# Optimization experiments

Measured on AMD Instinct MI355X. Metric: run time of the kernel, lower is better.

The kernel has to match this reference:

```python
import jax, jax.numpy as jnp
import numpy as np

SEQ_LEN = 4096
INPUT_DIM = 768
DIM = 512
NUM_HEADS = 8
HEAD_DIM = DIM // NUM_HEADS
WINDOW_SIZE = 7
DILATION = 8
HALF_WINDOW = WINDOW_SIZE // 2  # 3
BIDIRECTIONAL = True


def _dilated_mask(seq_len):
    # allowed neighbors of query i: j = i + k*DILATION for k in [-HALF_WINDOW, HALF_WINDOW]
    # (only k<=0 if not bidirectional), clipped to [0, seq_len)
    idx = jnp.arange(seq_len)
    d = idx[None, :] - idx[:, None]  # j - i
    allowed = (d % DILATION == 0) & (jnp.abs(d) <= DILATION * HALF_WINDOW)
    if not BIDIRECTIONAL:
        allowed = allowed & (d <= 0)
    return jnp.where(allowed, 0.0, -jnp.inf).astype(jnp.float32)  # [S, S]


def setup_inputs() -> dict:
    key = jax.random.key(0)
    ks = jax.random.split(key, 6)
    s = 0.02
    return {
        "x": jax.random.normal(ks[0], (SEQ_LEN, INPUT_DIM), dtype=jnp.float32),
        "W_in": jax.random.normal(ks[1], (INPUT_DIM, DIM), dtype=jnp.float32) * s,
        "b_in": jnp.zeros((DIM,), dtype=jnp.float32),
        "W_tse": jax.random.normal(ks[2], (DIM, 3 * DIM), dtype=jnp.float32) * s,
        "W_out": jax.random.normal(ks[3], (DIM, DIM), dtype=jnp.float32) * s,
        "b_out": jnp.zeros((DIM,), dtype=jnp.float32),
    }


def reference(x, W_in, b_in, W_tse, W_out, b_out):
    S = x.shape[0]
    scale = HEAD_DIM ** -0.5
    h = x @ W_in + b_in                                   # [S, DIM]
    tse = (h @ W_tse).reshape(S, 3, NUM_HEADS, HEAD_DIM)   # [S, 3, H, hd]
    q, k, v = tse[:, 0], tse[:, 1], tse[:, 2]              # each [S, H, hd]
    scores = jnp.einsum("shd,thd->hst", q, k) * scale      # [H, S, S]
    scores = scores + _dilated_mask(S)[None, :, :]
    attn = jax.nn.softmax(scores, axis=-1)                 # [H, S, S]
    out = jnp.einsum("hst,thd->shd", attn, v)              # [S, H, hd]
    out = out.reshape(S, DIM)
    return out @ W_out + b_out                              # [S, DIM]
```

## Files before the change

kernel.cpp:

```cpp
#include <hip/hip_runtime.h>
#include <hip/hip_bf16.h>

#define S_LEN 4096
#define IN_DIM 768
#define D_DIM 512
#define N_HEADS 8
#define H_DIM 64
#define TSE_DIM 1536

typedef __attribute__((ext_vector_type(8))) short frag8;
typedef __attribute__((ext_vector_type(4))) float f32x4;

__device__ __forceinline__ unsigned short f2bfbits(float f) {
    unsigned int u = __float_as_uint(f);
    unsigned int r = (u + 0x7FFFu + ((u >> 16) & 1u)) >> 16;
    return (unsigned short)r;
}
__device__ __forceinline__ float bf2f(unsigned short b) {
    return __uint_as_float(((unsigned int)b) << 16);
}

__device__ __forceinline__ void gload_lds16(const void* g, void* l) {
    __builtin_amdgcn_global_load_lds(
        (const __attribute__((address_space(1))) unsigned int*)g,
        (__attribute__((address_space(3))) unsigned int*)l,
        16, 0, 0);
}

__global__ __launch_bounds__(256) void prep_kernel(
        const float4* __restrict__ x4, ushort4* __restrict__ xb4,
        const float* __restrict__ W_in,  unsigned short* __restrict__ WinT,
        const float* __restrict__ W_tse, unsigned short* __restrict__ WtseT,
        const float* __restrict__ W_out, unsigned short* __restrict__ WoutT) {
    __shared__ float tile[32][33];
    int b = blockIdx.x;
    if (b < 3072) {
        int i = b * 256 + threadIdx.x;
        float4 v = x4[i];
        ushort4 o;
        o.x = f2bfbits(v.x); o.y = f2bfbits(v.y);
        o.z = f2bfbits(v.z); o.w = f2bfbits(v.w);
        xb4[i] = o;
        return;
    }
    const float* in; unsigned short* out; int K, N, t;
    if (b < 3456)      { t = b - 3072; in = W_in;  out = WinT;  K = IN_DIM; N = D_DIM;  }
    else if (b < 4224) { t = b - 3456; in = W_tse; out = WtseT; K = D_DIM;  N = TSE_DIM;}
    else               { t = b - 4224; in = W_out; out = WoutT; K = D_DIM;  N = D_DIM;  }
    int ktiles = K / 32;
    int kb = (t % ktiles) * 32, nb = (t / ktiles) * 32;
    int tx = threadIdx.x & 31, ty = threadIdx.x >> 5;
    #pragma unroll
    for (int r = ty; r < 32; r += 8)
        tile[r][tx] = in[(size_t)(kb + r) * N + nb + tx];
    __syncthreads();
    #pragma unroll
    for (int r = ty; r < 32; r += 8)
        out[(size_t)(nb + r) * K + kb + tx] = f2bfbits(tile[tx][r]);
}

template<int K, bool OUT_BF16, bool BIAS>
__global__ __launch_bounds__(256) void gemm_nt(
        const unsigned short* __restrict__ A,
        const unsigned short* __restrict__ Bt,
        const float* __restrict__ bias,
        void* __restrict__ C,
        int M, int N) {
    constexpr int NT = K >> 5;
    constexpr int NP = NT >> 1;
    __shared__ __align__(16) unsigned short As[4][64 * 32];
    __shared__ __align__(16) unsigned short Bs[4][64 * 32];

    const int bm = blockIdx.x * 64;
    const int bn = blockIdx.y * 64;
    const int lane = threadIdx.x & 63;
    const int wave = threadIdx.x >> 6;
    const int wr = wave >> 1;
    const int wc = wave & 1;
    const int fr = lane & 15;
    const int fg = lane >> 4;

    const int srow = lane >> 2;
    const int scol = (lane & 3) * 8;

    const unsigned short* agp = A  + (size_t)(bm + wave * 16 + srow) * K + scol;
    const unsigned short* bgp = Bt + (size_t)(bn + wave * 16 + srow) * K + scol;

    f32x4 acc[2][2];
    #pragma unroll
    for (int mi = 0; mi < 2; ++mi)
        #pragma unroll
        for (int ni = 0; ni < 2; ++ni)
            acc[mi][ni] = (f32x4)(0.f);

    #define STAGE(t, b)                                          \
        gload_lds16(agp + (t) * 32, &As[b][wave * 512]);         \
        gload_lds16(bgp + (t) * 32, &Bs[b][wave * 512]);

    #define COMPUTE(b)                                                           \
        {                                                                        \
            frag8 a_[2], b_[2];                                                  \
            _Pragma("unroll")                                                    \
            for (int mi = 0; mi < 2; ++mi)                                       \
                a_[mi] = *(const frag8*)&As[b][(wr * 32 + mi * 16 + fr) * 32 + fg * 8]; \
            _Pragma("unroll")                                                    \
            for (int ni = 0; ni < 2; ++ni)                                       \
                b_[ni] = *(const frag8*)&Bs[b][(wc * 32 + ni * 16 + fr) * 32 + fg * 8]; \
            _Pragma("unroll")                                                    \
            for (int mi = 0; mi < 2; ++mi)                                       \
                _Pragma("unroll")                                                \
                for (int ni = 0; ni < 2; ++ni)                                   \
                    acc[mi][ni] = __builtin_amdgcn_mfma_f32_16x16x32_bf16(       \
                            a_[mi], b_[ni], acc[mi][ni], 0, 0, 0);               \
        }

    STAGE(0, 0)
    STAGE(1, 1)
    __syncthreads();

    #pragma unroll
    for (int p = 0; p < NP; ++p) {
        const int s0 = (p & 1) * 2;
        if (p + 1 < NP) {
            const int s1 = ((p + 1) & 1) * 2;
            STAGE(2 * p + 2, s1 + 0)
            STAGE(2 * p + 3, s1 + 1)
        }
        COMPUTE(s0 + 0)
        COMPUTE(s0 + 1)
        if (p + 1 < NP) __syncthreads();
    }
    #undef STAGE
    #undef COMPUTE

    #pragma unroll
    for (int mi = 0; mi < 2; ++mi) {
        int grow = bm + wr * 32 + mi * 16 + fg * 4;
        #pragma unroll
        for (int ni = 0; ni < 2; ++ni) {
            int gcol = bn + wc * 32 + ni * 16 + fr;
            float bv = BIAS ? bias[gcol] : 0.f;
            #pragma unroll
            for (int r = 0; r < 4; ++r) {
                float v = acc[mi][ni][r] + bv;
                if (OUT_BF16)
                    ((unsigned short*)C)[(size_t)(grow + r) * N + gcol] = f2bfbits(v);
                else
                    ((float*)C)[(size_t)(grow + r) * N + gcol] = v;
            }
        }
    }
}

__global__ __launch_bounds__(256) void attn_kernel(
        const unsigned short* __restrict__ tse, unsigned short* __restrict__ out) {
    const int s    = blockIdx.x * 4 + (threadIdx.x >> 6);
    const int lane = threadIdx.x & 63;
    const int off  = (lane >> 3) * H_DIM + (lane & 7) * 8;

    float qf[8];
    {
        frag8 q = *(const frag8*)(tse + (size_t)s * TSE_DIM + off);
        #pragma unroll
        for (int i = 0; i < 8; ++i) qf[i] = bf2f((unsigned short)q[i]);
    }

    float sc[7];
    #pragma unroll
    for (int j = 0; j < 7; ++j) {
        int t = s + (j - 3) * 8;
        bool valid = (t >= 0) && (t < S_LEN);
        float p = 0.f;
        if (valid) {
            frag8 k = *(const frag8*)(tse + (size_t)t * TSE_DIM + D_DIM + off);
            #pragma unroll
            for (int i = 0; i < 8; ++i) p += qf[i] * bf2f((unsigned short)k[i]);
        }
        p += __shfl_xor(p, 1, 64);
        p += __shfl_xor(p, 2, 64);
        p += __shfl_xor(p, 4, 64);
        sc[j] = valid ? p * 0.125f : -__builtin_inff();
    }

    float m = sc[0];
    #pragma unroll
    for (int j = 1; j < 7; ++j) m = fmaxf(m, sc[j]);

    float w[7], denom = 0.f;
    #pragma unroll
    for (int j = 0; j < 7; ++j) {
        w[j] = (sc[j] == -__builtin_inff()) ? 0.f : __expf(sc[j] - m);
        denom += w[j];
    }
    const float inv = 1.f / denom;

    float of[8];
    #pragma unroll
    for (int i = 0; i < 8; ++i) of[i] = 0.f;
    #pragma unroll
    for (int j = 0; j < 7; ++j) {
        int t = s + (j - 3) * 8;
        if (t >= 0 && t < S_LEN) {
            frag8 v = *(const frag8*)(tse + (size_t)t * TSE_DIM + 2 * D_DIM + off);
            #pragma unroll
            for (int i = 0; i < 8; ++i) of[i] += w[j] * bf2f((unsigned short)v[i]);
        }
    }

    frag8 o;
    #pragma unroll
    for (int i = 0; i < 8; ++i) o[i] = (short)f2bfbits(of[i] * inv);
    *(frag8*)(out + (size_t)s * D_DIM + off) = o;
}

extern "C" void kernel_launch(void* const* d_in, const int* in_sizes, int n_in,
                              void* d_out, int out_size, void* d_ws, size_t ws_size,
                              hipStream_t stream) {
    (void)in_sizes; (void)n_in; (void)out_size;
    const float* x     = (const float*)d_in[0];
    const float* W_in  = (const float*)d_in[1];
    const float* b_in  = (const float*)d_in[2];
    const float* W_tse = (const float*)d_in[3];
    const float* W_out = (const float*)d_in[4];
    const float* b_out = (const float*)d_in[5];

    char* p = (char*)d_ws;
    unsigned short* xb    = (unsigned short*)p; p += (size_t)S_LEN * IN_DIM * 2;
    unsigned short* WinT  = (unsigned short*)p; p += (size_t)D_DIM * IN_DIM * 2;
    unsigned short* WtseT = (unsigned short*)p; p += (size_t)TSE_DIM * D_DIM * 2;
    unsigned short* WoutT = (unsigned short*)p; p += (size_t)D_DIM * D_DIM * 2;
    unsigned short* h     = (unsigned short*)p; p += (size_t)S_LEN * D_DIM * 2;
    unsigned short* tse   = (unsigned short*)p; p += (size_t)S_LEN * TSE_DIM * 2;
    unsigned short* attn  = (unsigned short*)p; p += (size_t)S_LEN * D_DIM * 2;
    if ((size_t)(p - (char*)d_ws) > ws_size) return;

    prep_kernel<<<4480, 256, 0, stream>>>(
            (const float4*)x, (ushort4*)xb, W_in, WinT, W_tse, WtseT, W_out, WoutT);

    gemm_nt<IN_DIM, true, true><<<dim3(S_LEN / 64, D_DIM / 64), 256, 0, stream>>>(
            xb, WinT, b_in, h, S_LEN, D_DIM);
    gemm_nt<D_DIM, true, false><<<dim3(S_LEN / 64, TSE_DIM / 64), 256, 0, stream>>>(
            h, WtseT, nullptr, tse, S_LEN, TSE_DIM);
    attn_kernel<<<S_LEN / 4, 256, 0, stream>>>(tse, attn);
    gemm_nt<D_DIM, false, true><<<dim3(S_LEN / 64, D_DIM / 64), 256, 0, stream>>>(
            attn, WoutT, b_out, (float*)d_out, S_LEN, D_DIM);
}
```

Measured before the change: 56.65 us.

## Pre-pack weights into MFMA fragment layout and load B directly to registers

The prep kernel now writes each weight matrix in a packed 16x32 MFMA-fragment order, so every lane can read its B operand straight from global memory with one 16-byte load. The GEMM drops the B shared-memory staging and keeps only a double-buffered A tile. It also moves from processing two K-tiles per barrier to a single K-tile per step with register prefetch of the next B fragments. This removes LDS traffic and LDS space for B, but adds a barrier per K step and makes the B loads depend on global/L2 latency being hidden.

```diff
diff --git a/kernel.cpp b/kernel.cpp
--- a/kernel.cpp
+++ b/kernel.cpp
@@ -29,9 +29,9 @@
 
 __global__ __launch_bounds__(256) void prep_kernel(
         const float4* __restrict__ x4, ushort4* __restrict__ xb4,
-        const float* __restrict__ W_in,  unsigned short* __restrict__ WinT,
-        const float* __restrict__ W_tse, unsigned short* __restrict__ WtseT,
-        const float* __restrict__ W_out, unsigned short* __restrict__ WoutT) {
+        const float* __restrict__ W_in,  unsigned short* __restrict__ WinP,
+        const float* __restrict__ W_tse, unsigned short* __restrict__ WtseP,
+        const float* __restrict__ W_out, unsigned short* __restrict__ WoutP) {
     __shared__ float tile[32][33];
     int b = blockIdx.x;
     if (b < 3072) {
@@ -44,32 +44,36 @@
         return;
     }
     const float* in; unsigned short* out; int K, N, t;
-    if (b < 3456)      { t = b - 3072; in = W_in;  out = WinT;  K = IN_DIM; N = D_DIM;  }
-    else if (b < 4224) { t = b - 3456; in = W_tse; out = WtseT; K = D_DIM;  N = TSE_DIM;}
-    else               { t = b - 4224; in = W_out; out = WoutT; K = D_DIM;  N = D_DIM;  }
-    int ktiles = K / 32;
-    int kb = (t % ktiles) * 32, nb = (t / ktiles) * 32;
-    int tx = threadIdx.x & 31, ty = threadIdx.x >> 5;
+    if (b < 3456)      { t = b - 3072; in = W_in;  out = WinP;  K = IN_DIM; N = D_DIM;  }
+    else if (b < 4224) { t = b - 3456; in = W_tse; out = WtseP; K = D_DIM;  N = TSE_DIM;}
+    else               { t = b - 4224; in = W_out; out = WoutP; K = D_DIM;  N = D_DIM;  }
+    const int ktiles = K / 32;
+    const int kb = (t % ktiles) * 32, nb = (t / ktiles) * 32;
+    const int tx = threadIdx.x & 31, ty = threadIdx.x >> 5;
     #pragma unroll
     for (int r = ty; r < 32; r += 8)
         tile[r][tx] = in[(size_t)(kb + r) * N + nb + tx];
     __syncthreads();
-    #pragma unroll
-    for (int r = ty; r < 32; r += 8)
-        out[(size_t)(nb + r) * K + kb + tx] = f2bfbits(tile[tx][r]);
+    if (threadIdx.x < 128) {
+        const int g = threadIdx.x >> 6;
+        const int l = threadIdx.x & 63;
+        frag8 o;
+        #pragma unroll
+        for (int j = 0; j < 8; ++j)
+            o[j] = (short)f2bfbits(tile[(l >> 4) * 8 + j][g * 16 + (l & 15)]);
+        *(frag8*)(out + ((size_t)(nb / 16 + g) * ktiles + kb / 32) * 512 + (size_t)l * 8) = o;
+    }
 }
 
 template<int K, bool OUT_BF16, bool BIAS>
-__global__ __launch_bounds__(256) void gemm_nt(
+__global__ __launch_bounds__(256) void gemm_bp(
         const unsigned short* __restrict__ A,
-        const unsigned short* __restrict__ Bt,
+        const unsigned short* __restrict__ Bp,
         const float* __restrict__ bias,
         void* __restrict__ C,
         int M, int N) {
     constexpr int NT = K >> 5;
-    constexpr int NP = NT >> 1;
-    __shared__ __align__(16) unsigned short As[4][64 * 32];
-    __shared__ __align__(16) unsigned short Bs[4][64 * 32];
+    __shared__ __align__(16) unsigned short As[2][64 * 32];
 
     const int bm = blockIdx.x * 64;
     const int bn = blockIdx.y * 64;
@@ -79,12 +83,14 @@
     const int wc = wave & 1;
     const int fr = lane & 15;
     const int fg = lane >> 4;
-
     const int srow = lane >> 2;
     const int scol = (lane & 3) * 8;
 
-    const unsigned short* agp = A  + (size_t)(bm + wave * 16 + srow) * K + scol;
-    const unsigned short* bgp = Bt + (size_t)(bn + wave * 16 + srow) * K + scol;
+    const unsigned short* agp = A + (size_t)(bm + wave * 16 + srow) * K + scol;
+    const unsigned short* bb0 =
+        Bp + ((size_t)((bn >> 4) + wc * 2 + 0) * NT) * 512 + lane * 8;
+    const unsigned short* bb1 =
+        Bp + ((size_t)((bn >> 4) + wc * 2 + 1) * NT) * 512 + lane * 8;
 
     f32x4 acc[2][2];
     #pragma unroll
@@ -93,45 +99,34 @@
         for (int ni = 0; ni < 2; ++ni)
             acc[mi][ni] = (f32x4)(0.f);
 
-    #define STAGE(t, b)                                          \
-        gload_lds16(agp + (t) * 32, &As[b][wave * 512]);         \
-        gload_lds16(bgp + (t) * 32, &Bs[b][wave * 512]);
-
-    #define COMPUTE(b)                                                           \
-        {                                                                        \
-            frag8 a_[2], b_[2];                                                  \
-            _Pragma("unroll")                                                    \
-            for (int mi = 0; mi < 2; ++mi)                                       \
-                a_[mi] = *(const frag8*)&As[b][(wr * 32 + mi * 16 + fr) * 32 + fg * 8]; \
-            _Pragma("unroll")                                                    \
-            for (int ni = 0; ni < 2; ++ni)                                       \
-                b_[ni] = *(const frag8*)&Bs[b][(wc * 32 + ni * 16 + fr) * 32 + fg * 8]; \
-            _Pragma("unroll")                                                    \
-            for (int mi = 0; mi < 2; ++mi)                                       \
-                _Pragma("unroll")                                                \
-                for (int ni = 0; ni < 2; ++ni)                                   \
-                    acc[mi][ni] = __builtin_amdgcn_mfma_f32_16x16x32_bf16(       \
-                            a_[mi], b_[ni], acc[mi][ni], 0, 0, 0);               \
-        }
-
-    STAGE(0, 0)
-    STAGE(1, 1)
+    gload_lds16(agp, &As[0][wave * 512]);
+    frag8 bc0 = *(const frag8*)bb0;
+    frag8 bc1 = *(const frag8*)bb1;
     __syncthreads();
 
-    #pragma unroll
-    for (int p = 0; p < NP; ++p) {
-        const int s0 = (p & 1) * 2;
-        if (p + 1 < NP) {
-            const int s1 = ((p + 1) & 1) * 2;
-            STAGE(2 * p + 2, s1 + 0)
-            STAGE(2 * p + 3, s1 + 1)
-        }
-        COMPUTE(s0 + 0)
-        COMPUTE(s0 + 1)
-        if (p + 1 < NP) __syncthreads();
-    }
-    #undef STAGE
-    #undef COMPUTE
+    int cur = 0;
+    #pragma unroll
+    for (int kt = 0; kt < NT; ++kt) {
+        frag8 bq0, bq1;
+        if (kt + 1 < NT) {
+            gload_lds16(agp + (kt + 1) * 32, &As[cur ^ 1][wave * 512]);
+            bq0 = *(const frag8*)(bb0 + (size_t)(kt + 1) * 512);
+            bq1 = *(const frag8*)(bb1 + (size_t)(kt + 1) * 512);
+        }
+
+        frag8 a0 = *(const frag8*)&As[cur][(wr * 32 + 0  + fr) * 32 + fg * 8];
+        frag8 a1 = *(const frag8*)&As[cur][(wr * 32 + 16 + fr) * 32 + fg * 8];
+        acc[0][0] = __builtin_amdgcn_mfma_f32_16x16x32_bf16(a0, bc0, acc[0][0], 0, 0, 0);
+        acc[0][1] = __builtin_amdgcn_mfma_f32_16x16x32_bf16(a0, bc1, acc[0][1], 0, 0, 0);
+        acc[1][0] = __builtin_amdgcn_mfma_f32_16x16x32_bf16(a1, bc0, acc[1][0], 0, 0, 0);
+        acc[1][1] = __builtin_amdgcn_mfma_f32_16x16x32_bf16(a1, bc1, acc[1][1], 0, 0, 0);
+
+        if (kt + 1 < NT) {
+            __syncthreads();
+            cur ^= 1;
+            bc0 = bq0; bc1 = bq1;
+        }
+    }
 
     #pragma unroll
     for (int mi = 0; mi < 2; ++mi) {
@@ -226,22 +221,22 @@
 
     char* p = (char*)d_ws;
     unsigned short* xb    = (unsigned short*)p; p += (size_t)S_LEN * IN_DIM * 2;
-    unsigned short* WinT  = (unsigned short*)p; p += (size_t)D_DIM * IN_DIM * 2;
-    unsigned short* WtseT = (unsigned short*)p; p += (size_t)TSE_DIM * D_DIM * 2;
-    unsigned short* WoutT = (unsigned short*)p; p += (size_t)D_DIM * D_DIM * 2;
+    unsigned short* WinP  = (unsigned short*)p; p += (size_t)IN_DIM * D_DIM * 2;
+    unsigned short* WtseP = (unsigned short*)p; p += (size_t)D_DIM * TSE_DIM * 2;
+    unsigned short* WoutP = (unsigned short*)p; p += (size_t)D_DIM * D_DIM * 2;
     unsigned short* h     = (unsigned short*)p; p += (size_t)S_LEN * D_DIM * 2;
     unsigned short* tse   = (unsigned short*)p; p += (size_t)S_LEN * TSE_DIM * 2;
     unsigned short* attn  = (unsigned short*)p; p += (size_t)S_LEN * D_DIM * 2;
     if ((size_t)(p - (char*)d_ws) > ws_size) return;
 
     prep_kernel<<<4480, 256, 0, stream>>>(
-            (const float4*)x, (ushort4*)xb, W_in, WinT, W_tse, WtseT, W_out, WoutT);
-
-    gemm_nt<IN_DIM, true, true><<<dim3(S_LEN / 64, D_DIM / 64), 256, 0, stream>>>(
-            xb, WinT, b_in, h, S_LEN, D_DIM);
-    gemm_nt<D_DIM, true, false><<<dim3(S_LEN / 64, TSE_DIM / 64), 256, 0, stream>>>(
-            h, WtseT, nullptr, tse, S_LEN, TSE_DIM);
+            (const float4*)x, (ushort4*)xb, W_in, WinP, W_tse, WtseP, W_out, WoutP);
+
+    gemm_bp<IN_DIM, true, true><<<dim3(S_LEN / 64, D_DIM / 64), 256, 0, stream>>>(
+            xb, WinP, b_in, h, S_LEN, D_DIM);
+    gemm_bp<D_DIM, true, false><<<dim3(S_LEN / 64, TSE_DIM / 64), 256, 0, stream>>>(
+            h, WtseP, nullptr, tse, S_LEN, TSE_DIM);
     attn_kernel<<<S_LEN / 4, 256, 0, stream>>>(tse, attn);
-    gemm_nt<D_DIM, false, true><<<dim3(S_LEN / 64, D_DIM / 64), 256, 0, stream>>>(
-            attn, WoutT, b_out, (float*)d_out, S_LEN, D_DIM);
-}
+    gemm_bp<D_DIM, false, true><<<dim3(S_LEN / 64, D_DIM / 64), 256, 0, stream>>>(
+            attn, WoutP, b_out, (float*)d_out, S_LEN, D_DIM);
+}
```

New measurement: 56.25 us. About the same (-0.7%).
